# Kernel optimization log

Hardware: AMD Instinct MI355X
Metric: run time of the kernel (lower is better)

Reference implementation:

```python
import jax, jax.numpy as jnp
import numpy as np

E = 8          # num_experts
K = 2          # top_k
CAPF = 1.25    # capacity_factor


def setup_inputs() -> dict:
    key = jax.random.key(0)
    ks = jax.random.split(key, 6)
    B, T, C = 4, 2048, 1024
    x = jax.random.normal(ks[0], (B, T, C), jnp.float32)
    noise = jax.random.normal(ks[1], (B, T, E), jnp.float32)  # stands in for torch.randn_like
    Wr = jax.random.normal(ks[2], (C, E), jnp.float32) * 0.02   # topkroute_linear
    Wn = jax.random.normal(ks[3], (C, E), jnp.float32) * 0.02   # noise_linear
    W1 = jax.random.normal(ks[4], (E, C, 4 * C), jnp.float32) * 0.02  # expert up-proj
    W2 = jax.random.normal(ks[5], (E, 4 * C, C), jnp.float32) * 0.02  # expert down-proj
    return {"x": x, "noise": noise, "Wr": Wr, "Wn": Wn, "W1": W1, "W2": W2}


def reference(x, noise, Wr, Wn, W1, W2):
    B, T, C = x.shape
    N = B * T
    cap = int(N * K / E * CAPF)  # expert_capacity (static)

    # --- NoisyTopkRouter ---
    logits = x @ Wr                                  # [B,T,E]
    noise_logits = x @ Wn                            # [B,T,E]
    noisy = logits + noise * jax.nn.softplus(noise_logits)
    _, idx = jax.lax.top_k(noisy, K)                 # [B,T,K]
    mask_bte = (idx[..., None] == jnp.arange(E)).any(axis=-2)       # [B,T,E]
    gating = jax.nn.softmax(jnp.where(mask_bte, noisy, -jnp.inf), axis=-1)

    flat_x = x.reshape(N, C)
    flat_g = gating.reshape(N, E)

    # --- capacity-limited dispatch (token order, first `cap` per expert) ---
    mask = mask_bte.reshape(N, E).T                  # [E,N]
    rank = jnp.cumsum(mask, axis=1) - 1              # position within expert
    keep = mask & (rank < cap)
    slot = jnp.where(keep, rank, cap)                # overflow -> dump slot `cap`
    tok = jnp.where(keep, jnp.arange(N)[None, :], N) # dropped -> pad token `N`
    s2t = jnp.full((E, cap + 1), N, dtype=jnp.int32)
    s2t = s2t.at[jnp.arange(E)[:, None], slot].set(tok.astype(jnp.int32))[:, :cap]  # [E,cap]

    # --- gather, grouped GEMM (Linear-SiLU-Linear), weight, scatter-add ---
    x_pad = jnp.concatenate([flat_x, jnp.zeros((1, C), flat_x.dtype)], axis=0)
    xin = x_pad[s2t]                                 # [E,cap,C]
    h = jax.nn.silu(jnp.einsum('enc,ech->enh', xin, W1))
    out = jnp.einsum('enh,ehc->enc', h, W2)          # [E,cap,C]
    g_pad = jnp.concatenate([flat_g, jnp.zeros((1, E), flat_g.dtype)], axis=0)
    gate = g_pad[s2t, jnp.arange(E)[:, None]]        # [E,cap]
    weighted = out * gate[..., None]
    upd = jnp.zeros((N + 1, C), x.dtype).at[s2t.reshape(-1)].add(weighted.reshape(-1, C))
    return upd[:N].reshape(B, T, C)
```

## Files before the change

### kernel.cpp

```cpp
#include <hip/hip_runtime.h>
#include <hip/hip_bf16.h>
#include <math.h>

#define C_DIM 1024
#define H_DIM 4096
#define E_NUM 8

typedef __bf16 bf16x8 __attribute__((ext_vector_type(8)));
typedef float f32x4 __attribute__((ext_vector_type(4)));

__device__ __forceinline__ unsigned short f2bf(float f) {
  union { float f; unsigned u; } v; v.f = f;
  unsigned r = v.u + 0x7FFFu + ((v.u >> 16) & 1u);
  return (unsigned short)(r >> 16);
}

__device__ __forceinline__ void gload16(const short* g, short* l) {
  __builtin_amdgcn_global_load_lds(
      (const __attribute__((address_space(1))) unsigned int*)g,
      (__attribute__((address_space(3))) unsigned int*)l, 16, 0, 0);
}

__global__ __launch_bounds__(256) void router_kernel(
    const float* __restrict__ x, const float* __restrict__ noise,
    const float* __restrict__ Wr, const float* __restrict__ Wn,
    int2* __restrict__ idx_out, float2* __restrict__ gate_out, int N)
{
  int t = blockIdx.x;
  int tid = threadIdx.x;
  const float* xrow = x + (size_t)t * C_DIM;
  float accR[E_NUM], accN[E_NUM];
#pragma unroll
  for (int e = 0; e < E_NUM; e++) { accR[e] = 0.f; accN[e] = 0.f; }
  for (int c = tid; c < C_DIM; c += 256) {
    float xv = xrow[c];
    const float* wr = Wr + (size_t)c * E_NUM;
    const float* wn = Wn + (size_t)c * E_NUM;
#pragma unroll
    for (int e = 0; e < E_NUM; e++) {
      accR[e] = fmaf(xv, wr[e], accR[e]);
      accN[e] = fmaf(xv, wn[e], accN[e]);
    }
  }
#pragma unroll
  for (int e = 0; e < E_NUM; e++) {
    for (int off = 32; off > 0; off >>= 1) {
      accR[e] += __shfl_down(accR[e], off, 64);
      accN[e] += __shfl_down(accN[e], off, 64);
    }
  }
  __shared__ float red[4][2 * E_NUM];
  int lane = tid & 63, wave = tid >> 6;
  if (lane == 0) {
#pragma unroll
    for (int e = 0; e < E_NUM; e++) { red[wave][e] = accR[e]; red[wave][E_NUM + e] = accN[e]; }
  }
  __syncthreads();
  if (tid == 0) {
    float ns[E_NUM];
#pragma unroll
    for (int e = 0; e < E_NUM; e++) {
      float lg = red[0][e] + red[1][e] + red[2][e] + red[3][e];
      float nl = red[0][E_NUM + e] + red[1][E_NUM + e] + red[2][E_NUM + e] + red[3][E_NUM + e];
      float sp = fmaxf(nl, 0.f) + log1pf(expf(-fabsf(nl)));
      ns[e] = lg + noise[(size_t)t * E_NUM + e] * sp;
    }
    int i1 = 0; float m1 = ns[0];
    int i2 = -1; float m2 = -INFINITY;
#pragma unroll
    for (int e = 1; e < E_NUM; e++) {
      float v = ns[e];
      if (v > m1) { m2 = m1; i2 = i1; m1 = v; i1 = e; }
      else if (v > m2) { m2 = v; i2 = e; }
    }
    float e2 = expf(m2 - m1);
    float s = 1.f + e2;
    gate_out[t] = make_float2(1.f / s, e2 / s);
    idx_out[t] = make_int2(i1, i2);
  }
}

__global__ __launch_bounds__(256) void scan_kernel(
    const int2* __restrict__ idx, const float2* __restrict__ gates,
    int* __restrict__ s2t, float* __restrict__ gslot, int* __restrict__ counts,
    int N, int cap)
{
  int e = blockIdx.x;
  int tid = threadIdx.x;
  for (int s = tid; s < cap; s += 256) { s2t[(size_t)e * cap + s] = N; gslot[(size_t)e * cap + s] = 0.f; }
  __syncthreads();
  __shared__ int wtot[4];
  int lane = tid & 63, wave = tid >> 6;
  int running = 0;
  for (int base = 0; base < N; base += 256) {
    int t = base + tid;
    int2 ix = idx[t];
    bool flag = (ix.x == e) || (ix.y == e);
    unsigned long long m = __ballot(flag);
    int rank = __popcll(m & ((1ull << lane) - 1ull));
    if (lane == 0) wtot[wave] = __popcll(m);
    __syncthreads();
    int woff = 0;
    for (int w = 0; w < wave; w++) woff += wtot[w];
    int slot = running + woff + rank;
    if (flag && slot < cap) {
      s2t[(size_t)e * cap + slot] = t;
      gslot[(size_t)e * cap + slot] = (ix.x == e) ? gates[t].x : gates[t].y;
    }
    running += wtot[0] + wtot[1] + wtot[2] + wtot[3];
    __syncthreads();
  }
  if (tid == 0) counts[e] = min(running, cap);
}

__global__ __launch_bounds__(256) void convert_x_kernel(
    const float* __restrict__ src, short* __restrict__ dst, int n8)
{
  int i = blockIdx.x * 256 + threadIdx.x;
  if (i >= n8) return;
  const float4* s = (const float4*)src + (size_t)i * 2;
  float4 a = s[0], b = s[1];
  union { unsigned short us[8]; uint4 v; } o;
  o.us[0] = f2bf(a.x); o.us[1] = f2bf(a.y); o.us[2] = f2bf(a.z); o.us[3] = f2bf(a.w);
  o.us[4] = f2bf(b.x); o.us[5] = f2bf(b.y); o.us[6] = f2bf(b.z); o.us[7] = f2bf(b.w);
  ((uint4*)dst)[i] = o.v;
}

__global__ __launch_bounds__(256) void transpose_convert_kernel(
    const float* __restrict__ src, short* __restrict__ dst,
    int R, int Cc)
{
  src += (size_t)blockIdx.z * R * Cc;
  dst += (size_t)blockIdx.z * (size_t)R * Cc;
  __shared__ float tile[64][65];
  int c0 = blockIdx.x * 64, r0 = blockIdx.y * 64;
  int tid = threadIdx.x;
  int tr = tid >> 4, tc = (tid & 15) * 4;
#pragma unroll
  for (int p = 0; p < 4; p++) {
    int r = p * 16 + tr;
    float4 v = *(const float4*)(src + (size_t)(r0 + r) * Cc + c0 + tc);
    tile[r][tc] = v.x; tile[r][tc + 1] = v.y; tile[r][tc + 2] = v.z; tile[r][tc + 3] = v.w;
  }
  __syncthreads();
#pragma unroll
  for (int p = 0; p < 4; p++) {
    int c = p * 16 + tr;
    union { unsigned short us[4]; ushort4 v; } o;
#pragma unroll
    for (int j = 0; j < 4; j++) o.us[j] = f2bf(tile[tc + j][c]);
    *(ushort4*)(dst + (size_t)(c0 + c) * R + r0 + tc) = o.v;
  }
}

#define TILE_SH 8192

template<int MODE>
__global__ __launch_bounds__(512, 2) void gemm_moe(
    const short* __restrict__ Abase, const short* __restrict__ Wt,
    const int* __restrict__ s2t, const float* __restrict__ gslot,
    const int* __restrict__ counts, void* __restrict__ outp,
    int cap, int N, int rows)
{
  __shared__ short As[4 * TILE_SH];
  __shared__ short Bs[4 * TILE_SH];

  int nwg = gridDim.x;
  int cpx = nwg >> 3;
  int flat = blockIdx.x;
  int swz = (flat & 7) * cpx + (flat >> 3);

  int row, col, e, kc;
  if (MODE == 0) {
    row = swz % rows; int tmp = swz / rows;
    col = tmp & 15; e = tmp >> 4; kc = 0;
  } else {
    row = swz % rows; int tmp = swz / rows;
    col = tmp & 3; tmp >>= 2;
    kc = tmp & 3; e = tmp >> 2;
  }
  int cnt = counts[e];
  int row0 = row * 256;
  if (row0 >= cnt) return;
  int col0 = col * 256;

  int tid = threadIdx.x;
  int w = tid >> 6, l = tid & 63;
  int wr = w >> 2, wc = w & 3;
  int srow = (w & 3) * 64 + l;
  int ko0 = (w >> 2) * 8;
  int ko1 = (2 + (w >> 2)) * 8;
  int ld0 = (w * 64 + l) * 8;
  int ld1 = (512 + w * 64 + l) * 8;

  const short* gA;
  const short* gB;
  if (MODE == 0) {
    int tok = s2t[(size_t)e * cap + row0 + srow];
    if (tok >= N) tok = N - 1;
    gA = Abase + (size_t)tok * C_DIM;
    gB = Wt + (size_t)e * (C_DIM * H_DIM) + (size_t)(col0 + srow) * C_DIM;
  } else {
    gA = Abase + ((size_t)e * cap + row0 + srow) * H_DIM + kc * 1024;
    gB = Wt + (size_t)e * (C_DIM * H_DIM) + (size_t)(col0 + srow) * H_DIM + kc * 1024;
  }
  const int KT = 32;

  int aBase = ((l >> 4) * 256 + wr * 128 + (l & 15)) * 8;
  int bBase = ((l >> 4) * 256 + wc * 64 + (l & 15)) * 8;

  f32x4 acc[8][4];
#pragma unroll
  for (int m = 0; m < 8; m++)
#pragma unroll
    for (int n = 0; n < 4; n++) acc[m][n] = 0.f;

#pragma unroll
  for (int t = 0; t < 3; ++t) {
    int boff = t * TILE_SH;
    gload16(gA + t * 32 + ko0, &As[boff + ld0]);
    gload16(gA + t * 32 + ko1, &As[boff + ld1]);
    gload16(gB + t * 32 + ko0, &Bs[boff + ld0]);
    gload16(gB + t * 32 + ko1, &Bs[boff + ld1]);
  }

#pragma unroll 1
  for (int t = 0; t < KT; ++t) {
    if (t < KT - 2)       asm volatile("s_waitcnt vmcnt(8)" ::: "memory");
    else if (t == KT - 2) asm volatile("s_waitcnt vmcnt(4)" ::: "memory");
    else                  asm volatile("s_waitcnt vmcnt(0)" ::: "memory");
    __builtin_amdgcn_s_barrier();
    __builtin_amdgcn_sched_barrier(0);

    int bufc = (t & 3) * TILE_SH;
    int tp = t + 3;
    int bufp = (tp & 3) * TILE_SH;
    bool st = tp < KT;

    if (st) {
      gload16(gA + tp * 32 + ko0, &As[bufp + ld0]);
      gload16(gA + tp * 32 + ko1, &As[bufp + ld1]);
    }
    bf16x8 bfr[4], afr[4];
#pragma unroll
    for (int n = 0; n < 4; n++) bfr[n] = *(const bf16x8*)&Bs[bufc + bBase + n * 128];
#pragma unroll
    for (int m = 0; m < 4; m++) afr[m] = *(const bf16x8*)&As[bufc + aBase + m * 128];
    __builtin_amdgcn_s_setprio(1);
#pragma unroll
    for (int m = 0; m < 4; m++)
#pragma unroll
      for (int n = 0; n < 4; n++)
        acc[m][n] = __builtin_amdgcn_mfma_f32_16x16x32_bf16(afr[m], bfr[n], acc[m][n], 0, 0, 0);
    __builtin_amdgcn_s_setprio(0);

    if (st) {
      gload16(gB + tp * 32 + ko0, &Bs[bufp + ld0]);
      gload16(gB + tp * 32 + ko1, &Bs[bufp + ld1]);
    }
#pragma unroll
    for (int m = 0; m < 4; m++) afr[m] = *(const bf16x8*)&As[bufc + aBase + (m + 4) * 128];
    __builtin_amdgcn_s_setprio(1);
#pragma unroll
    for (int m = 0; m < 4; m++)
#pragma unroll
      for (int n = 0; n < 4; n++)
        acc[m + 4][n] = __builtin_amdgcn_mfma_f32_16x16x32_bf16(afr[m], bfr[n], acc[m + 4][n], 0, 0, 0);
    __builtin_amdgcn_s_setprio(0);
  }

  int orow = row0 + wr * 128 + (l >> 4) * 4;
  int ocol = col0 + wc * 64 + (l & 15);
  if (MODE == 0) {
    short* hE = (short*)outp + (size_t)e * cap * H_DIM;
#pragma unroll
    for (int m = 0; m < 8; m++)
#pragma unroll
      for (int r = 0; r < 4; r++) {
        size_t rb = (size_t)(orow + m * 16 + r) * H_DIM + ocol;
#pragma unroll
        for (int n = 0; n < 4; n++) {
          float v = acc[m][n][r];
          hE[rb + n * 16] = (short)f2bf(v / (1.f + expf(-v)));
        }
      }
  } else {
    float* out = (float*)outp;
#pragma unroll
    for (int m = 0; m < 8; m++)
#pragma unroll
      for (int r = 0; r < 4; r++) {
        int slot = row0 + wr * 128 + m * 16 + (l >> 4) * 4 + r;
        int tok = s2t[(size_t)e * cap + slot];
        if (tok < N) {
          float g = gslot[(size_t)e * cap + slot];
          float* op = out + (size_t)tok * C_DIM + ocol;
#pragma unroll
          for (int n = 0; n < 4; n++)
            atomicAdd(op + n * 16, g * acc[m][n][r]);
        }
      }
  }
}

extern "C" void kernel_launch(void* const* d_in, const int* in_sizes, int n_in,
                              void* d_out, int out_size, void* d_ws, size_t ws_size,
                              hipStream_t stream)
{
  const float* x     = (const float*)d_in[0];
  const float* noise = (const float*)d_in[1];
  const float* Wr    = (const float*)d_in[2];
  const float* Wn    = (const float*)d_in[3];
  const float* W1    = (const float*)d_in[4];
  const float* W2    = (const float*)d_in[5];
  float* out = (float*)d_out;

  int N = in_sizes[0] / C_DIM;
  int cap = (int)((double)N * 2.0 / E_NUM * 1.25);
  int rows = cap / 256;

  size_t off = 0;
  auto alloc = [&](size_t bytes) -> char* {
    char* r = (char*)d_ws + off;
    off += (bytes + 255) & ~(size_t)255;
    return r;
  };
  int2*   idx    = (int2*)alloc((size_t)N * sizeof(int2));
  float2* gates  = (float2*)alloc((size_t)N * sizeof(float2));
  int*    s2t    = (int*)alloc((size_t)E_NUM * cap * sizeof(int));
  float*  gslot  = (float*)alloc((size_t)E_NUM * cap * sizeof(float));
  int*    counts = (int*)alloc(E_NUM * sizeof(int));
  short*  xbf    = (short*)alloc((size_t)N * C_DIM * sizeof(short));
  short*  W1t    = (short*)alloc((size_t)E_NUM * C_DIM * H_DIM * sizeof(short));
  short*  W2t    = (short*)alloc((size_t)E_NUM * C_DIM * H_DIM * sizeof(short));
  short*  h      = (short*)alloc((size_t)E_NUM * cap * H_DIM * sizeof(short));
  (void)ws_size;

  hipMemsetAsync(d_out, 0, (size_t)out_size * sizeof(float), stream);
  router_kernel<<<N, 256, 0, stream>>>(x, noise, Wr, Wn, idx, gates, N);
  scan_kernel<<<E_NUM, 256, 0, stream>>>(idx, gates, s2t, gslot, counts, N, cap);
  convert_x_kernel<<<(N * C_DIM / 8 + 255) / 256, 256, 0, stream>>>(x, xbf, N * C_DIM / 8);
  transpose_convert_kernel<<<dim3(H_DIM / 64, C_DIM / 64, E_NUM), 256, 0, stream>>>(
      W1, W1t, C_DIM, H_DIM);
  transpose_convert_kernel<<<dim3(C_DIM / 64, H_DIM / 64, E_NUM), 256, 0, stream>>>(
      W2, W2t, H_DIM, C_DIM);

  gemm_moe<0><<<dim3(16 * rows * E_NUM), 512, 0, stream>>>(
      xbf, W1t, s2t, gslot, counts, h, cap, N, rows);
  gemm_moe<1><<<dim3(4 * rows * 4 * E_NUM), 512, 0, stream>>>(
      h, W2t, s2t, gslot, counts, out, cap, N, rows);
}
```

Baseline: 865.7 us.

## Restructure MoE GEMM mainloop into 8-wave ping-pong schedule with K=64 half-tiles

```diff
diff --git a/kernel.cpp b/kernel.cpp
--- a/kernel.cpp
+++ b/kernel.cpp
@@ -8,6 +8,7 @@
 
 typedef __bf16 bf16x8 __attribute__((ext_vector_type(8)));
 typedef float f32x4 __attribute__((ext_vector_type(4)));
+typedef unsigned u32x4 __attribute__((ext_vector_type(4)));
 
 __device__ __forceinline__ unsigned short f2bf(float f) {
   union { float f; unsigned u; } v; v.f = f;
@@ -20,6 +21,20 @@
       (const __attribute__((address_space(1))) unsigned int*)g,
       (__attribute__((address_space(3))) unsigned int*)l, 16, 0, 0);
 }
+
+__device__ __forceinline__ f32x4 mfma16(u32x4 a, u32x4 b, f32x4 c) {
+  return __builtin_amdgcn_mfma_f32_16x16x32_bf16(
+      __builtin_bit_cast(bf16x8, a), __builtin_bit_cast(bf16x8, b), c, 0, 0, 0);
+}
+
+#define DSR(v, a, imm) asm volatile("ds_read_b128 %0, %1 offset:" #imm : "=v"(v) : "v"(a))
+#define BAR __builtin_amdgcn_s_barrier()
+#define LGKM0 { asm volatile("s_waitcnt lgkmcnt(0)" ::: "memory"); __builtin_amdgcn_sched_barrier(0); }
+#define VMW(n) asm volatile("s_waitcnt vmcnt(" #n ")" ::: "memory")
+#define SP1 __builtin_amdgcn_s_setprio(1)
+#define SP0 __builtin_amdgcn_s_setprio(0)
+#define STG(p, d) { gload16((p), (d)); gload16((p) + 32, (d) + 4096); }
+#define LDS_U32(p) ((unsigned)(size_t)(__attribute__((address_space(3))) short*)(p))
 
 __global__ __launch_bounds__(256) void router_kernel(
     const float* __restrict__ x, const float* __restrict__ noise,
@@ -153,8 +168,6 @@
   }
 }
 
-#define TILE_SH 8192
-
 template<int MODE>
 __global__ __launch_bounds__(512, 2) void gemm_moe(
     const short* __restrict__ Abase, const short* __restrict__ Wt,
@@ -162,8 +175,8 @@
     const int* __restrict__ counts, void* __restrict__ outp,
     int cap, int N, int rows)
 {
-  __shared__ short As[4 * TILE_SH];
-  __shared__ short Bs[4 * TILE_SH];
+  __shared__ short As[32768];
+  __shared__ short Bs[32768];
 
   int nwg = gridDim.x;
   int cpx = nwg >> 3;
@@ -187,27 +200,30 @@
   int tid = threadIdx.x;
   int w = tid >> 6, l = tid & 63;
   int wr = w >> 2, wc = w & 3;
-  int srow = (w & 3) * 64 + l;
-  int ko0 = (w >> 2) * 8;
-  int ko1 = (2 + (w >> 2)) * 8;
-  int ld0 = (w * 64 + l) * 8;
-  int ld1 = (512 + w * 64 + l) * 8;
-
-  const short* gA;
-  const short* gB;
+
+  int rowT = tid & 127;
+  int kbT = tid >> 7;
+  int kb8 = kbT * 8;
+  int dOff = kbT * 1024 + rowT * 8;
+
+  const short *pA0, *pA1, *pB0, *pB1;
   if (MODE == 0) {
-    int tok = s2t[(size_t)e * cap + row0 + srow];
-    if (tok >= N) tok = N - 1;
-    gA = Abase + (size_t)tok * C_DIM;
-    gB = Wt + (size_t)e * (C_DIM * H_DIM) + (size_t)(col0 + srow) * C_DIM;
+    int tok0 = min(s2t[(size_t)e * cap + row0 + rowT], N - 1);
+    int tok1 = min(s2t[(size_t)e * cap + row0 + 128 + rowT], N - 1);
+    pA0 = Abase + (size_t)tok0 * C_DIM;
+    pA1 = Abase + (size_t)tok1 * C_DIM;
+    pB0 = Wt + (size_t)e * (C_DIM * H_DIM) + (size_t)(col0 + rowT) * C_DIM;
+    pB1 = Wt + (size_t)e * (C_DIM * H_DIM) + (size_t)(col0 + 128 + rowT) * C_DIM;
   } else {
-    gA = Abase + ((size_t)e * cap + row0 + srow) * H_DIM + kc * 1024;
-    gB = Wt + (size_t)e * (C_DIM * H_DIM) + (size_t)(col0 + srow) * H_DIM + kc * 1024;
-  }
-  const int KT = 32;
-
-  int aBase = ((l >> 4) * 256 + wr * 128 + (l & 15)) * 8;
-  int bBase = ((l >> 4) * 256 + wc * 64 + (l & 15)) * 8;
+    pA0 = Abase + ((size_t)e * cap + row0 + rowT) * H_DIM + kc * 1024;
+    pA1 = Abase + ((size_t)e * cap + row0 + 128 + rowT) * H_DIM + kc * 1024;
+    pB0 = Wt + (size_t)e * (C_DIM * H_DIM) + (size_t)(col0 + rowT) * H_DIM + kc * 1024;
+    pB1 = Wt + (size_t)e * (C_DIM * H_DIM) + (size_t)(col0 + 128 + rowT) * H_DIM + kc * 1024;
+  }
+
+  unsigned aB0 = LDS_U32(As) + (unsigned)(wr * 16384 + (l >> 4) * 2048 + (l & 15) * 16);
+  unsigned bB0 = LDS_U32(Bs) + (unsigned)((wc >> 1) * 16384 + (l >> 4) * 2048 + ((wc & 1) * 64 + (l & 15)) * 16);
+  unsigned aB1 = aB0 + 32768, bB1 = bB0 + 32768;
 
   f32x4 acc[8][4];
 #pragma unroll
@@ -215,58 +231,74 @@
 #pragma unroll
     for (int n = 0; n < 4; n++) acc[m][n] = 0.f;
 
-#pragma unroll
-  for (int t = 0; t < 3; ++t) {
-    int boff = t * TILE_SH;
-    gload16(gA + t * 32 + ko0, &As[boff + ld0]);
-    gload16(gA + t * 32 + ko1, &As[boff + ld1]);
-    gload16(gB + t * 32 + ko0, &Bs[boff + ld0]);
-    gload16(gB + t * 32 + ko1, &Bs[boff + ld1]);
-  }
-
+  u32x4 aF0[4], aF1[4];
+  u32x4 bA[2], bB[2], bC[2], bD[2];
+
+#define RD_A(aa) { DSR(aF0[0],(aa),0); DSR(aF0[1],(aa),256); DSR(aF0[2],(aa),512); DSR(aF0[3],(aa),768); \
+                   DSR(aF1[0],(aa),8192); DSR(aF1[1],(aa),8448); DSR(aF1[2],(aa),8704); DSR(aF1[3],(aa),8960); }
+#define RD_BN0(bb) { DSR(bA[0],(bb),0); DSR(bA[1],(bb),256); DSR(bB[0],(bb),8192); DSR(bB[1],(bb),8448); }
+#define RD_BN1(bb) { DSR(bC[0],(bb),512); DSR(bC[1],(bb),768); DSR(bD[0],(bb),8704); DSR(bD[1],(bb),8960); }
+#define QUAD(MH, NH, F0, F1) { SP1; \
+  _Pragma("unroll") for (int mm = 0; mm < 4; mm++) \
+    _Pragma("unroll") for (int nn = 0; nn < 2; nn++) { \
+      acc[(MH)*4+mm][(NH)*2+nn] = mfma16(aF0[mm], F0[nn], acc[(MH)*4+mm][(NH)*2+nn]); \
+      acc[(MH)*4+mm][(NH)*2+nn] = mfma16(aF1[mm], F1[nn], acc[(MH)*4+mm][(NH)*2+nn]); \
+    } SP0; }
+
+  STG(pB0 + kb8,      Bs + dOff);
+  STG(pA0 + kb8,      As + dOff);
+  STG(pA1 + kb8,      As + 8192 + dOff);
+  STG(pB1 + kb8,      Bs + 8192 + dOff);
+  STG(pB0 + 64 + kb8, Bs + 16384 + dOff);
+  STG(pA0 + 64 + kb8, As + 16384 + dOff);
+  VMW(4); BAR;
+
+  const int NIT = 8;
 #pragma unroll 1
-  for (int t = 0; t < KT; ++t) {
-    if (t < KT - 2)       asm volatile("s_waitcnt vmcnt(8)" ::: "memory");
-    else if (t == KT - 2) asm volatile("s_waitcnt vmcnt(4)" ::: "memory");
-    else                  asm volatile("s_waitcnt vmcnt(0)" ::: "memory");
-    __builtin_amdgcn_s_barrier();
-    __builtin_amdgcn_sched_barrier(0);
-
-    int bufc = (t & 3) * TILE_SH;
-    int tp = t + 3;
-    int bufp = (tp & 3) * TILE_SH;
-    bool st = tp < KT;
-
-    if (st) {
-      gload16(gA + tp * 32 + ko0, &As[bufp + ld0]);
-      gload16(gA + tp * 32 + ko1, &As[bufp + ld1]);
-    }
-    bf16x8 bfr[4], afr[4];
-#pragma unroll
-    for (int n = 0; n < 4; n++) bfr[n] = *(const bf16x8*)&Bs[bufc + bBase + n * 128];
-#pragma unroll
-    for (int m = 0; m < 4; m++) afr[m] = *(const bf16x8*)&As[bufc + aBase + m * 128];
-    __builtin_amdgcn_s_setprio(1);
-#pragma unroll
-    for (int m = 0; m < 4; m++)
-#pragma unroll
-      for (int n = 0; n < 4; n++)
-        acc[m][n] = __builtin_amdgcn_mfma_f32_16x16x32_bf16(afr[m], bfr[n], acc[m][n], 0, 0, 0);
-    __builtin_amdgcn_s_setprio(0);
-
-    if (st) {
-      gload16(gB + tp * 32 + ko0, &Bs[bufp + ld0]);
-      gload16(gB + tp * 32 + ko1, &Bs[bufp + ld1]);
-    }
-#pragma unroll
-    for (int m = 0; m < 4; m++) afr[m] = *(const bf16x8*)&As[bufc + aBase + (m + 4) * 128];
-    __builtin_amdgcn_s_setprio(1);
-#pragma unroll
-    for (int m = 0; m < 4; m++)
-#pragma unroll
-      for (int n = 0; n < 4; n++)
-        acc[m + 4][n] = __builtin_amdgcn_mfma_f32_16x16x32_bf16(afr[m], bfr[n], acc[m + 4][n], 0, 0, 0);
-    __builtin_amdgcn_s_setprio(0);
+  for (int i = 0; i < NIT; ++i) {
+    bool lastI = (i == NIT - 1);
+    int t1k = (2 * i + 1) * 64, t2k = (2 * i + 2) * 64, t3k = (2 * i + 3) * 64;
+
+    RD_A(aB0); RD_BN0(bB0);
+    STG(pA1 + t1k + kb8, As + 16384 + 8192 + dOff);
+    BAR; LGKM0;
+    QUAD(0, 0, bA, bB);
+    BAR;
+    RD_BN1(bB0);
+    STG(pB1 + t1k + kb8, Bs + 16384 + 8192 + dOff);
+    BAR; LGKM0;
+    QUAD(0, 1, bC, bD);
+    BAR;
+    RD_A(aB0 + 1024);
+    if (!lastI) STG(pB0 + t2k + kb8, Bs + dOff);
+    BAR; LGKM0;
+    QUAD(1, 1, bC, bD);
+    BAR;
+    if (!lastI) STG(pA0 + t2k + kb8, As + dOff);
+    BAR;
+    QUAD(1, 0, bA, bB);
+    if (lastI) { VMW(0); } else { VMW(4); }
+    BAR;
+    RD_A(aB1); RD_BN0(bB1);
+    if (!lastI) STG(pA1 + t2k + kb8, As + 8192 + dOff);
+    BAR; LGKM0;
+    QUAD(0, 0, bA, bB);
+    BAR;
+    RD_BN1(bB1);
+    if (!lastI) STG(pB1 + t2k + kb8, Bs + 8192 + dOff);
+    BAR; LGKM0;
+    QUAD(0, 1, bC, bD);
+    BAR;
+    RD_A(aB1 + 1024);
+    if (!lastI) STG(pB0 + t3k + kb8, Bs + 16384 + dOff);
+    BAR; LGKM0;
+    QUAD(1, 1, bC, bD);
+    BAR;
+    if (!lastI) STG(pA0 + t3k + kb8, As + 16384 + dOff);
+    BAR;
+    QUAD(1, 0, bA, bB);
+    VMW(4);
+    BAR;
   }
 
   int orow = row0 + wr * 128 + (l >> 4) * 4;
@@ -301,6 +333,10 @@
         }
       }
   }
+#undef RD_A
+#undef RD_BN0
+#undef RD_BN1
+#undef QUAD
 }
 
 extern "C" void kernel_launch(void* const* d_in, const int* in_sizes, int n_in,
```

New measurement: 784.3 us. 9.4% less time.

## Rewrite grouped GEMM with 128x128 tiles, double buffering, and no split-K

Applied to the files above, without the earlier changes.

```diff
diff --git a/kernel.cpp b/kernel.cpp
--- a/kernel.cpp
+++ b/kernel.cpp
@@ -153,128 +153,90 @@
   }
 }
 
-#define TILE_SH 8192
-
 template<int MODE>
-__global__ __launch_bounds__(512, 2) void gemm_moe(
+__global__ __launch_bounds__(256, 2) void gemm_moe(
     const short* __restrict__ Abase, const short* __restrict__ Wt,
     const int* __restrict__ s2t, const float* __restrict__ gslot,
     const int* __restrict__ counts, void* __restrict__ outp,
-    int cap, int N, int rows)
-{
-  __shared__ short As[4 * TILE_SH];
-  __shared__ short Bs[4 * TILE_SH];
-
-  int nwg = gridDim.x;
-  int cpx = nwg >> 3;
-  int flat = blockIdx.x;
-  int swz = (flat & 7) * cpx + (flat >> 3);
-
-  int row, col, e, kc;
-  if (MODE == 0) {
-    row = swz % rows; int tmp = swz / rows;
-    col = tmp & 15; e = tmp >> 4; kc = 0;
-  } else {
-    row = swz % rows; int tmp = swz / rows;
-    col = tmp & 3; tmp >>= 2;
-    kc = tmp & 3; e = tmp >> 2;
-  }
+    int cap, int N)
+{
+  __shared__ short As[2][8192];
+  __shared__ short Bs[2][8192];
+
+  int e = blockIdx.z;
   int cnt = counts[e];
-  int row0 = row * 256;
+  int row0 = blockIdx.y * 128;
   if (row0 >= cnt) return;
-  int col0 = col * 256;
+  int col0 = blockIdx.x * 128;
 
   int tid = threadIdx.x;
   int w = tid >> 6, l = tid & 63;
-  int wr = w >> 2, wc = w & 3;
-  int srow = (w & 3) * 64 + l;
-  int ko0 = (w >> 2) * 8;
-  int ko1 = (2 + (w >> 2)) * 8;
-  int ld0 = (w * 64 + l) * 8;
-  int ld1 = (512 + w * 64 + l) * 8;
-
-  const short* gA;
-  const short* gB;
+  int wr = w >> 1, wc = w & 1;
+  int rowT = tid & 127, kbT = tid >> 7;
+
+  constexpr int KS = (MODE == 0) ? C_DIM : H_DIM;
+  constexpr int NS = KS / 64;
+
+  const short *pA, *pB;
   if (MODE == 0) {
-    int tok = s2t[(size_t)e * cap + row0 + srow];
-    if (tok >= N) tok = N - 1;
-    gA = Abase + (size_t)tok * C_DIM;
-    gB = Wt + (size_t)e * (C_DIM * H_DIM) + (size_t)(col0 + srow) * C_DIM;
+    int tok = min(s2t[e * cap + row0 + rowT], N - 1);
+    pA = Abase + (size_t)tok * C_DIM;
+    pB = Wt + (size_t)e * (C_DIM * H_DIM) + (size_t)(col0 + rowT) * C_DIM;
   } else {
-    gA = Abase + ((size_t)e * cap + row0 + srow) * H_DIM + kc * 1024;
-    gB = Wt + (size_t)e * (C_DIM * H_DIM) + (size_t)(col0 + srow) * H_DIM + kc * 1024;
-  }
-  const int KT = 32;
-
-  int aBase = ((l >> 4) * 256 + wr * 128 + (l & 15)) * 8;
-  int bBase = ((l >> 4) * 256 + wc * 64 + (l & 15)) * 8;
-
-  f32x4 acc[8][4];
-#pragma unroll
-  for (int m = 0; m < 8; m++)
+    pA = Abase + ((size_t)e * cap + row0 + rowT) * H_DIM;
+    pB = Wt + (size_t)e * (C_DIM * H_DIM) + (size_t)(col0 + rowT) * H_DIM;
+  }
+
+  int aBase = (l >> 4) * 1024 + (wr * 64 + (l & 15)) * 8;
+  int bBase = (l >> 4) * 1024 + (wc * 64 + (l & 15)) * 8;
+
+  f32x4 acc[4][4];
+#pragma unroll
+  for (int m = 0; m < 4; m++)
 #pragma unroll
     for (int n = 0; n < 4; n++) acc[m][n] = 0.f;
 
-#pragma unroll
-  for (int t = 0; t < 3; ++t) {
-    int boff = t * TILE_SH;
-    gload16(gA + t * 32 + ko0, &As[boff + ld0]);
-    gload16(gA + t * 32 + ko1, &As[boff + ld1]);
-    gload16(gB + t * 32 + ko0, &Bs[boff + ld0]);
-    gload16(gB + t * 32 + ko1, &Bs[boff + ld1]);
-  }
-
+#define STAGE(k0, buf) { \
+  _Pragma("unroll") for (int j = 0; j < 4; ++j) { \
+    int kb = kbT + 2 * j; \
+    gload16(pA + (k0) + kb * 8, &As[buf][kb * 1024 + rowT * 8]); \
+    gload16(pB + (k0) + kb * 8, &Bs[buf][kb * 1024 + rowT * 8]); \
+  } }
+
+  STAGE(0, 0);
+  int cur = 0;
 #pragma unroll 1
-  for (int t = 0; t < KT; ++t) {
-    if (t < KT - 2)       asm volatile("s_waitcnt vmcnt(8)" ::: "memory");
-    else if (t == KT - 2) asm volatile("s_waitcnt vmcnt(4)" ::: "memory");
-    else                  asm volatile("s_waitcnt vmcnt(0)" ::: "memory");
-    __builtin_amdgcn_s_barrier();
-    __builtin_amdgcn_sched_barrier(0);
-
-    int bufc = (t & 3) * TILE_SH;
-    int tp = t + 3;
-    int bufp = (tp & 3) * TILE_SH;
-    bool st = tp < KT;
-
-    if (st) {
-      gload16(gA + tp * 32 + ko0, &As[bufp + ld0]);
-      gload16(gA + tp * 32 + ko1, &As[bufp + ld1]);
-    }
-    bf16x8 bfr[4], afr[4];
-#pragma unroll
-    for (int n = 0; n < 4; n++) bfr[n] = *(const bf16x8*)&Bs[bufc + bBase + n * 128];
-#pragma unroll
-    for (int m = 0; m < 4; m++) afr[m] = *(const bf16x8*)&As[bufc + aBase + m * 128];
-    __builtin_amdgcn_s_setprio(1);
+  for (int i = 0; i < NS; ++i) {
+    __syncthreads();
+    bf16x8 af[4][2], bg[4][2];
 #pragma unroll
     for (int m = 0; m < 4; m++)
 #pragma unroll
-      for (int n = 0; n < 4; n++)
-        acc[m][n] = __builtin_amdgcn_mfma_f32_16x16x32_bf16(afr[m], bfr[n], acc[m][n], 0, 0, 0);
-    __builtin_amdgcn_s_setprio(0);
-
-    if (st) {
-      gload16(gB + tp * 32 + ko0, &Bs[bufp + ld0]);
-      gload16(gB + tp * 32 + ko1, &Bs[bufp + ld1]);
-    }
-#pragma unroll
-    for (int m = 0; m < 4; m++) afr[m] = *(const bf16x8*)&As[bufc + aBase + (m + 4) * 128];
-    __builtin_amdgcn_s_setprio(1);
+      for (int kk = 0; kk < 2; kk++)
+        af[m][kk] = *(const bf16x8*)&As[cur][aBase + m * 128 + kk * 4096];
+#pragma unroll
+    for (int n = 0; n < 4; n++)
+#pragma unroll
+      for (int kk = 0; kk < 2; kk++)
+        bg[n][kk] = *(const bf16x8*)&Bs[cur][bBase + n * 128 + kk * 4096];
+    if (i + 1 < NS) STAGE((i + 1) * 64, cur ^ 1);
 #pragma unroll
     for (int m = 0; m < 4; m++)
 #pragma unroll
-      for (int n = 0; n < 4; n++)
-        acc[m + 4][n] = __builtin_amdgcn_mfma_f32_16x16x32_bf16(afr[m], bfr[n], acc[m + 4][n], 0, 0, 0);
-    __builtin_amdgcn_s_setprio(0);
-  }
-
-  int orow = row0 + wr * 128 + (l >> 4) * 4;
+      for (int n = 0; n < 4; n++) {
+        acc[m][n] = __builtin_amdgcn_mfma_f32_16x16x32_bf16(af[m][0], bg[n][0], acc[m][n], 0, 0, 0);
+        acc[m][n] = __builtin_amdgcn_mfma_f32_16x16x32_bf16(af[m][1], bg[n][1], acc[m][n], 0, 0, 0);
+      }
+    cur ^= 1;
+  }
+#undef STAGE
+
+  int orow = row0 + wr * 64 + (l >> 4) * 4;
   int ocol = col0 + wc * 64 + (l & 15);
   if (MODE == 0) {
     short* hE = (short*)outp + (size_t)e * cap * H_DIM;
 #pragma unroll
-    for (int m = 0; m < 8; m++)
+    for (int m = 0; m < 4; m++)
 #pragma unroll
       for (int r = 0; r < 4; r++) {
         size_t rb = (size_t)(orow + m * 16 + r) * H_DIM + ocol;
@@ -287,13 +249,13 @@
   } else {
     float* out = (float*)outp;
 #pragma unroll
-    for (int m = 0; m < 8; m++)
+    for (int m = 0; m < 4; m++)
 #pragma unroll
       for (int r = 0; r < 4; r++) {
-        int slot = row0 + wr * 128 + m * 16 + (l >> 4) * 4 + r;
-        int tok = s2t[(size_t)e * cap + slot];
+        int slot = row0 + wr * 64 + m * 16 + (l >> 4) * 4 + r;
+        int tok = s2t[e * cap + slot];
         if (tok < N) {
-          float g = gslot[(size_t)e * cap + slot];
+          float g = gslot[e * cap + slot];
           float* op = out + (size_t)tok * C_DIM + ocol;
 #pragma unroll
           for (int n = 0; n < 4; n++)
@@ -317,7 +279,7 @@
 
   int N = in_sizes[0] / C_DIM;
   int cap = (int)((double)N * 2.0 / E_NUM * 1.25);
-  int rows = cap / 256;
+  int rows = cap / 128;
 
   size_t off = 0;
   auto alloc = [&](size_t bytes) -> char* {
@@ -345,8 +307,8 @@
   transpose_convert_kernel<<<dim3(C_DIM / 64, H_DIM / 64, E_NUM), 256, 0, stream>>>(
       W2, W2t, H_DIM, C_DIM);
 
-  gemm_moe<0><<<dim3(16 * rows * E_NUM), 512, 0, stream>>>(
-      xbf, W1t, s2t, gslot, counts, h, cap, N, rows);
-  gemm_moe<1><<<dim3(4 * rows * 4 * E_NUM), 512, 0, stream>>>(
-      h, W2t, s2t, gslot, counts, out, cap, N, rows);
-}
+  gemm_moe<0><<<dim3(H_DIM / 128, rows, E_NUM), 256, 0, stream>>>(
+      xbf, W1t, s2t, gslot, counts, h, cap, N);
+  gemm_moe<1><<<dim3(C_DIM / 128, rows, E_NUM), 256, 0, stream>>>(
+      h, W2t, s2t, gslot, counts, out, cap, N);
+}
```

New measurement: 936.8 us. 8.2% more time.
